# Optimization experiments

Measured on AMD Instinct MI355X. Metric: run time of the kernel, lower is better.

The kernel has to match this reference:

```python
import jax, jax.numpy as jnp
import numpy as np

EMB = 1024
HEADS = 16
HEAD_DIM = EMB // HEADS


def setup_inputs() -> dict:
    key = jax.random.key(0)
    ks = jax.random.split(key, 11)
    B, S = 2, 2048
    scale = 1.0 / np.sqrt(EMB)
    inp = {
        "query": jax.random.normal(ks[0], (B, S, EMB), jnp.float32),
        "key": jax.random.normal(ks[1], (B, S, EMB), jnp.float32),
        "value": jax.random.normal(ks[2], (B, S, EMB), jnp.float32),
        "Wq": jax.random.normal(ks[3], (EMB, EMB), jnp.float32) * scale,
        "bq": jnp.zeros((EMB,), jnp.float32),
        "Wk": jax.random.normal(ks[4], (EMB, EMB), jnp.float32) * scale,
        "bk": jnp.zeros((EMB,), jnp.float32),
        "Wv": jax.random.normal(ks[5], (EMB, EMB), jnp.float32) * scale,
        "bv": jnp.zeros((EMB,), jnp.float32),
        "Wo": jax.random.normal(ks[6], (EMB, EMB), jnp.float32) * scale,
        "bo": jnp.zeros((EMB,), jnp.float32),
    }
    return inp


def reference(query, key, value, Wq, bq, Wk, bk, Wv, bv, Wo, bo):
    B, S, _ = query.shape
    # Linear projections (torch Linear: x @ W.T + b)
    Q = query @ Wq.T + bq
    K = key @ Wk.T + bk
    V = value @ Wv.T + bv
    # [B, H, S, Dh]
    Q = Q.reshape(B, S, HEADS, HEAD_DIM).transpose(0, 2, 1, 3)
    K = K.reshape(B, S, HEADS, HEAD_DIM).transpose(0, 2, 1, 3)
    V = V.reshape(B, S, HEADS, HEAD_DIM).transpose(0, 2, 1, 3)
    scores = jnp.einsum("bhqd,bhkd->bhqk", Q, K) / jnp.sqrt(
        jnp.asarray(HEAD_DIM, Q.dtype)
    )
    attn = jax.nn.softmax(scores, axis=-1)
    ctx = jnp.einsum("bhqk,bhkd->bhqd", attn, V)
    ctx = ctx.transpose(0, 2, 1, 3).reshape(B, S, EMB)
    return ctx @ Wo.T + bo
```

## Files before the change

### kernel.cpp

```cpp
#include <hip/hip_runtime.h>
#include <stdint.h>

typedef __attribute__((ext_vector_type(8)))  __bf16 bf16x8;
typedef __attribute__((ext_vector_type(4)))  float  f32x4;
typedef __attribute__((ext_vector_type(16))) float  f32x16;
typedef __attribute__((ext_vector_type(8)))  ushort u16x8;
typedef __attribute__((ext_vector_type(4)))  ushort u16x4;
typedef __attribute__((ext_vector_type(4)))  uint   u32x4;

#define LOG2E 1.44269504088896f

__device__ __forceinline__ ushort f2bf(float f) {
  uint32_t u = __float_as_uint(f);
  u += 0x7fffu + ((u >> 16) & 1u);
  return (ushort)(u >> 16);
}
__device__ __forceinline__ float bf2f(ushort h) {
  return __uint_as_float(((uint32_t)h) << 16);
}
__device__ __forceinline__ void gload16(const void* g, void* l) {
  __builtin_amdgcn_global_load_lds((const __attribute__((address_space(1))) void*)g,
                                   (__attribute__((address_space(3))) void*)l, 16, 0, 0);
}
__device__ __forceinline__ f32x4 mfma16(bf16x8 a, bf16x8 b, f32x4 c) {
  return __builtin_amdgcn_mfma_f32_16x16x32_bf16(a, b, c, 0, 0, 0);
}
__device__ __forceinline__ f32x16 mfma32(bf16x8 a, bf16x8 b, f32x16 c) {
  return __builtin_amdgcn_mfma_f32_32x32x16_bf16(a, b, c, 0, 0, 0);
}
__device__ __forceinline__ int swz(int row, int byteoff) {
  return row * 128 + (byteoff ^ ((row & 7) << 4));
}
__device__ __forceinline__ uint cvtpk(float lo, float hi) {
  uint w;
  asm("v_cvt_pk_bf16_f32 %0, %1, %2" : "=v"(w) : "v"(lo), "v"(hi));
  return w;
}
__device__ __forceinline__ void plswap(uint& a, uint& b) {
  asm("v_permlane32_swap_b32 %0, %1" : "+v"(a), "+v"(b));
}

struct CvtArgs { const float* src[7]; ushort* dst[7]; };

__global__ __launch_bounds__(256) void cvt_all(CvtArgs a) {
  const int bid = blockIdx.x;
  int seg, base;
  if (bid < 2048) { seg = bid >> 9;              base = bid & 511; }
  else            { seg = 4 + ((bid - 2048) >> 11); base = (bid - 2048) & 2047; }
  const int i = base * 256 + threadIdx.x;
  const f32x4* s = (const f32x4*)a.src[seg];
  f32x4 x = s[2 * i], y = s[2 * i + 1];
  u16x8 o;
  o[0] = f2bf(x[0]); o[1] = f2bf(x[1]); o[2] = f2bf(x[2]); o[3] = f2bf(x[3]);
  o[4] = f2bf(y[0]); o[5] = f2bf(y[1]); o[6] = f2bf(y[2]); o[7] = f2bf(y[3]);
  ((u16x8*)a.dst[seg])[i] = o;
}

struct QKVArgs {
  const ushort* A0; const ushort* A1; const ushort* A2;
  const ushort* W0; const ushort* W1; const ushort* W2;
  const float* b0; const float* b1; const float* b2;
  ushort* Qo; ushort* Ko; ushort* Vo;
};

__global__ __launch_bounds__(256) void qkv_gemm(QKVArgs args) {
  __shared__ ushort Ash[128 * 64];
  __shared__ ushort Bsh[128 * 64];

  const int z = blockIdx.z;
  const ushort* Ab   = z == 0 ? args.A0 : (z == 1 ? args.A1 : args.A2);
  const ushort* Wb   = z == 0 ? args.W0 : (z == 1 ? args.W1 : args.W2);
  const float*  bias = z == 0 ? args.b0 : (z == 1 ? args.b1 : args.b2);

  const int tid = threadIdx.x;
  const int lane = tid & 63, wid = tid >> 6;
  const int l15 = lane & 15, g = lane >> 4;
  const int wr = wid >> 1, wc = wid & 1;
  const int tm = blockIdx.x * 128, tn = blockIdx.y * 128;

  const f32x4 fz = {0.f, 0.f, 0.f, 0.f};
  f32x4 acc[4][4];
#pragma unroll
  for (int m = 0; m < 4; ++m)
#pragma unroll
    for (int n = 0; n < 4; ++n) acc[m][n] = fz;

  const int srow8 = lane >> 3;
  const int ssl   = (lane & 7) ^ srow8;

  for (int kt = 0; kt < 1024; kt += 64) {
#pragma unroll
    for (int c = 0; c < 4; ++c) {
      const int chunk = wid * 4 + c;
      const int row = chunk * 8 + srow8;
      gload16(Wb + (size_t)(tn + row) * 1024 + kt + ssl * 8, &Bsh[chunk * 512]);
      gload16(Ab + (size_t)(tm + row) * 1024 + kt + ssl * 8, &Ash[chunk * 512]);
    }
    __syncthreads();

#pragma unroll
    for (int kk = 0; kk < 2; ++kk) {
      bf16x8 af[4], bfr[4];
#pragma unroll
      for (int m = 0; m < 4; ++m) {
        const int row = wr * 64 + m * 16 + l15;
        af[m] = *(const bf16x8*)&Ash[row * 64 + (((kk * 4 + g) ^ (row & 7)) * 8)];
      }
#pragma unroll
      for (int n = 0; n < 4; ++n) {
        const int row = wc * 64 + n * 16 + l15;
        bfr[n] = *(const bf16x8*)&Bsh[row * 64 + (((kk * 4 + g) ^ (row & 7)) * 8)];
      }
#pragma unroll
      for (int m = 0; m < 4; ++m)
#pragma unroll
        for (int n = 0; n < 4; ++n) acc[m][n] = mfma16(af[m], bfr[n], acc[m][n]);
    }
    __syncthreads();
  }

#pragma unroll
  for (int n = 0; n < 4; ++n) {
    const int col = tn + wc * 64 + n * 16 + l15;
    const float bv = bias[col];
    const int h = col >> 6, d = col & 63;
#pragma unroll
    for (int m = 0; m < 4; ++m) {
      const int row0 = tm + wr * 64 + m * 16 + g * 4;
      if (z == 2) {
        const int b = row0 >> 11, s0 = row0 & 2047;
        u16x4 pk;
#pragma unroll
        for (int r = 0; r < 4; ++r) pk[r] = f2bf(acc[m][n][r] + bv);
        *(u16x4*)&args.Vo[((size_t)((b * 16 + h) * 64 + d)) * 2048 + s0] = pk;
      } else {
        ushort* O = z ? args.Ko : args.Qo;
#pragma unroll
        for (int r = 0; r < 4; ++r) {
          const int row = row0 + r;
          const int b = row >> 11, s = row & 2047;
          O[((size_t)(b * 16 + h) * 2048 + s) * 64 + d] = f2bf(acc[m][n][r] + bv);
        }
      }
    }
  }
}

__global__ __launch_bounds__(256) void attn_fwd(const ushort* __restrict__ Qb,
                                                const ushort* __restrict__ Kb,
                                                const ushort* __restrict__ VTb,
                                                ushort* __restrict__ ctxb) {
  __shared__ char Ksh[64 * 128];
  __shared__ char Vsh[64 * 128];
  __shared__ float Ssc[4][32];

  const int tid = threadIdx.x;
  const int lane = tid & 63, wid = tid >> 6;
  const int l31 = lane & 31, hi = lane >> 5;
  const int bh = blockIdx.y;
  const int q0 = blockIdx.x * 128 + wid * 32;

  const ushort* Qh = Qb + (size_t)bh * 2048 * 64;
  const ushort* Kh = Kb + (size_t)bh * 2048 * 64;
  const ushort* Vh = VTb + (size_t)bh * 64 * 2048;

  bf16x8 qf[4];
  {
    const ushort* qrow = Qh + (size_t)(q0 + l31) * 64;
#pragma unroll
    for (int dt = 0; dt < 4; ++dt) {
      u16x8 raw = *(const u16x8*)&qrow[dt * 16 + hi * 8];
      u16x8 sc;
#pragma unroll
      for (int j = 0; j < 8; ++j) sc[j] = f2bf(bf2f(raw[j]) * 0.125f);
      qf[dt] = __builtin_bit_cast(bf16x8, sc);
    }
  }

  f32x16 o0 = {}, o1 = {};
  float m = -1e30f, lsum = 0.f;

  const int si = tid >> 2, sc4i = tid & 3;
  const ushort* kg = &Kh[(size_t)si * 64 + sc4i * 16];
  const ushort* vg = &Vh[(size_t)si * 2048 + sc4i * 16];

  u16x8 kr0, kr1, vr0, vr1;
  kr0 = *(const u16x8*)kg;  kr1 = *(const u16x8*)(kg + 8);
  vr0 = *(const u16x8*)vg;  vr1 = *(const u16x8*)(vg + 8);
  *(u16x8*)(Ksh + swz(si, sc4i * 32))      = kr0;
  *(u16x8*)(Ksh + swz(si, sc4i * 32 + 16)) = kr1;
  *(u16x8*)(Vsh + swz(si, sc4i * 32))      = vr0;
  *(u16x8*)(Vsh + swz(si, sc4i * 32 + 16)) = vr1;
  __syncthreads();

  for (int t = 0; t < 32; ++t) {
    if (t + 1 < 32) {
      const int kt2 = (t + 1) * 64;
      kr0 = *(const u16x8*)(kg + (size_t)kt2 * 64);
      kr1 = *(const u16x8*)(kg + (size_t)kt2 * 64 + 8);
      vr0 = *(const u16x8*)(vg + kt2);
      vr1 = *(const u16x8*)(vg + kt2 + 8);
    }

    f32x16 P0 = {}, P1 = {};
    __builtin_amdgcn_s_setprio(1);
#pragma unroll
    for (int dt = 0; dt < 4; ++dt) {
      bf16x8 kf0 = *(const bf16x8*)(Ksh + swz(l31,      dt * 32 + hi * 16));
      bf16x8 kf1 = *(const bf16x8*)(Ksh + swz(32 + l31, dt * 32 + hi * 16));
      P0 = mfma32(kf0, qf[dt], P0);
      P1 = mfma32(kf1, qf[dt], P1);
    }
    __builtin_amdgcn_s_setprio(0);

    float pm = fmaxf(P0[0], P1[0]);
#pragma unroll
    for (int r = 1; r + 1 < 16; r += 2) {
      pm = fmaxf(fmaxf(pm, P0[r]), P0[r + 1]);
      pm = fmaxf(fmaxf(pm, P1[r]), P1[r + 1]);
    }
    pm = fmaxf(fmaxf(pm, P0[15]), P1[15]);
    pm = fmaxf(pm, __shfl_xor(pm, 32));

    if (!__all(pm <= m + 8.f)) {
      const float mn = fmaxf(m, pm);
      const float scl = __builtin_amdgcn_exp2f((m - mn) * LOG2E);
      m = mn;
      lsum *= scl;
      Ssc[wid][l31] = scl;
      f32x4 s0 = *(const f32x4*)&Ssc[wid][hi * 4];
      f32x4 s1 = *(const f32x4*)&Ssc[wid][8 + hi * 4];
      f32x4 s2 = *(const f32x4*)&Ssc[wid][16 + hi * 4];
      f32x4 s3 = *(const f32x4*)&Ssc[wid][24 + hi * 4];
#pragma unroll
      for (int r = 0; r < 16; ++r) {
        const float sv = (r < 4 ? s0[r & 3] : r < 8 ? s1[r & 3] : r < 12 ? s2[r & 3] : s3[r & 3]);
        o0[r] *= sv; o1[r] *= sv;
      }
    }

    const float nml = -m * LOG2E;
#pragma unroll
    for (int r = 0; r < 16; ++r)
      P0[r] = __builtin_amdgcn_exp2f(__builtin_fmaf(P0[r], LOG2E, nml));
#pragma unroll
    for (int r = 0; r < 16; ++r)
      P1[r] = __builtin_amdgcn_exp2f(__builtin_fmaf(P1[r], LOG2E, nml));

    float rs = 0.f;
#pragma unroll
    for (int r = 0; r < 16; ++r) rs += P0[r] + P1[r];
    rs += __shfl_xor(rs, 32);
    lsum += rs;

    bf16x8 pa[4];
#pragma unroll
    for (int s = 0; s < 2; ++s) {
      const f32x16& P = s ? P1 : P0;
      uint a0 = cvtpk(P[0], P[1]),  b0 = cvtpk(P[4], P[5]);
      uint a1 = cvtpk(P[2], P[3]),  b1 = cvtpk(P[6], P[7]);
      plswap(a0, b0); plswap(a1, b1);
      pa[2 * s] = __builtin_bit_cast(bf16x8, (u32x4){a0, a1, b0, b1});
      uint a2 = cvtpk(P[8], P[9]),   b2 = cvtpk(P[12], P[13]);
      uint a3 = cvtpk(P[10], P[11]), b3 = cvtpk(P[14], P[15]);
      plswap(a2, b2); plswap(a3, b3);
      pa[2 * s + 1] = __builtin_bit_cast(bf16x8, (u32x4){a2, a3, b2, b3});
    }

    __builtin_amdgcn_s_setprio(1);
#pragma unroll
    for (int kk = 0; kk < 4; ++kk) {
      bf16x8 v0f = *(const bf16x8*)(Vsh + swz(l31,      kk * 32 + hi * 16));
      bf16x8 v1f = *(const bf16x8*)(Vsh + swz(32 + l31, kk * 32 + hi * 16));
      o0 = mfma32(pa[kk], v0f, o0);
      o1 = mfma32(pa[kk], v1f, o1);
    }
    __builtin_amdgcn_s_setprio(0);

    if (t + 1 < 32) {
      __syncthreads();
      *(u16x8*)(Ksh + swz(si, sc4i * 32))      = kr0;
      *(u16x8*)(Ksh + swz(si, sc4i * 32 + 16)) = kr1;
      *(u16x8*)(Vsh + swz(si, sc4i * 32))      = vr0;
      *(u16x8*)(Vsh + swz(si, sc4i * 32 + 16)) = vr1;
      __syncthreads();
    }
  }

  Ssc[wid][l31] = 1.0f / lsum;
  f32x4 i0 = *(const f32x4*)&Ssc[wid][hi * 4];
  f32x4 i1 = *(const f32x4*)&Ssc[wid][8 + hi * 4];
  f32x4 i2 = *(const f32x4*)&Ssc[wid][16 + hi * 4];
  f32x4 i3 = *(const f32x4*)&Ssc[wid][24 + hi * 4];
  const int b = bh >> 4, h = bh & 15;
#pragma unroll
  for (int r = 0; r < 16; ++r) {
    const float inv = (r < 4 ? i0[r & 3] : r < 8 ? i1[r & 3] : r < 12 ? i2[r & 3] : i3[r & 3]);
    const int q = q0 + (r & 3) + 8 * (r >> 2) + 4 * hi;
    const size_t base = ((size_t)(b * 2048 + q)) * 1024 + h * 64;
    ctxb[base + l31]      = f2bf(o0[r] * inv);
    ctxb[base + 32 + l31] = f2bf(o1[r] * inv);
  }
}

__global__ __launch_bounds__(256) void out_gemm(const ushort* __restrict__ A16,
                                                const ushort* __restrict__ Wb,
                                                const float* __restrict__ bias,
                                                float* __restrict__ O) {
  __shared__ ushort Ash[64 * 32];
  __shared__ ushort Bsh[128 * 32];

  const int tid = threadIdx.x;
  const int lane = tid & 63, wid = tid >> 6;
  const int l15 = lane & 15, g = lane >> 4;
  const int wr = wid >> 1, wc = wid & 1;
  const int tm = blockIdx.x * 64, tn = blockIdx.y * 128;

  const f32x4 fz = {0.f, 0.f, 0.f, 0.f};
  f32x4 acc[2][4];
#pragma unroll
  for (int m = 0; m < 2; ++m)
#pragma unroll
    for (int n = 0; n < 4; ++n) acc[m][n] = fz;

  for (int kt = 0; kt < 1024; kt += 32) {
#pragma unroll
    for (int c = 0; c < 2; ++c) {
      const int chunk = wid * 2 + c;
      const int off = chunk * 1024 + lane * 16;
      const int row = off >> 6;
      const int ke = (off & 63) >> 1;
      gload16(Wb + (size_t)(tn + row) * 1024 + kt + ke, &Bsh[chunk * 512]);
    }
    {
      const int off = wid * 1024 + lane * 16;
      const int row = off >> 6;
      const int ke = (off & 63) >> 1;
      gload16(A16 + (size_t)(tm + row) * 1024 + kt + ke, &Ash[wid * 512]);
    }
    __syncthreads();

    bf16x8 af[2], bfr[4];
#pragma unroll
    for (int m = 0; m < 2; ++m)
      af[m] = *(const bf16x8*)&Ash[(wr * 32 + m * 16 + l15) * 32 + g * 8];
#pragma unroll
    for (int n = 0; n < 4; ++n)
      bfr[n] = *(const bf16x8*)&Bsh[(wc * 64 + n * 16 + l15) * 32 + g * 8];
#pragma unroll
    for (int m = 0; m < 2; ++m)
#pragma unroll
      for (int n = 0; n < 4; ++n) acc[m][n] = mfma16(af[m], bfr[n], acc[m][n]);
    __syncthreads();
  }

#pragma unroll
  for (int n = 0; n < 4; ++n) {
    const int col = tn + wc * 64 + n * 16 + l15;
    const float bv = bias[col];
#pragma unroll
    for (int m = 0; m < 2; ++m) {
      const int row0 = tm + wr * 32 + m * 16 + g * 4;
#pragma unroll
      for (int r = 0; r < 4; ++r)
        O[(size_t)(row0 + r) * 1024 + col] = acc[m][n][r] + bv;
    }
  }
}

extern "C" void kernel_launch(void* const* d_in, const int* in_sizes, int n_in,
                              void* d_out, int out_size, void* d_ws, size_t ws_size,
                              hipStream_t stream) {
  const float* query = (const float*)d_in[0];
  const float* key_  = (const float*)d_in[1];
  const float* value = (const float*)d_in[2];
  const float* Wq = (const float*)d_in[3];
  const float* bq = (const float*)d_in[4];
  const float* Wk = (const float*)d_in[5];
  const float* bk = (const float*)d_in[6];
  const float* Wv = (const float*)d_in[7];
  const float* bv = (const float*)d_in[8];
  const float* Wo = (const float*)d_in[9];
  const float* bo = (const float*)d_in[10];

  ushort* ws = (ushort*)d_ws;
  ushort* Wqb = ws;
  ushort* Wkb = ws + (1u << 20);
  ushort* Wvb = ws + (2u << 20);
  ushort* Wob = ws + (3u << 20);
  ushort* Qb  = ws + (4u << 20);
  ushort* Kb  = Qb + (4u << 20);
  ushort* VTb = Kb + (4u << 20);
  ushort* ctx = VTb + (4u << 20);
  ushort* Xqb = ctx;
  ushort* Xkb = (ushort*)d_out;
  ushort* Xvb = (ushort*)d_out + (4u << 20);

  dim3 blk(256);

  CvtArgs ca;
  ca.src[0] = Wq;    ca.dst[0] = Wqb;
  ca.src[1] = Wk;    ca.dst[1] = Wkb;
  ca.src[2] = Wv;    ca.dst[2] = Wvb;
  ca.src[3] = Wo;    ca.dst[3] = Wob;
  ca.src[4] = query; ca.dst[4] = Xqb;
  ca.src[5] = key_;  ca.dst[5] = Xkb;
  ca.src[6] = value; ca.dst[6] = Xvb;
  cvt_all<<<8192, blk, 0, stream>>>(ca);

  QKVArgs a;
  a.A0 = Xqb;  a.A1 = Xkb;  a.A2 = Xvb;
  a.W0 = Wqb;  a.W1 = Wkb;  a.W2 = Wvb;
  a.b0 = bq;   a.b1 = bk;   a.b2 = bv;
  a.Qo = Qb;   a.Ko = Kb;   a.Vo = VTb;
  qkv_gemm<<<dim3(32, 8, 3), blk, 0, stream>>>(a);

  attn_fwd<<<dim3(16, 32), blk, 0, stream>>>(Qb, Kb, VTb, ctx);

  out_gemm<<<dim3(64, 8), blk, 0, stream>>>(ctx, Wob, bo, (float*)d_out);
}
```

Measured before the change: 136.1 us.

## Double-buffer K/V tiles in LDS with direct global-to-LDS async loads

Replaces the register-staged K/V prefetch with global_load_lds direct loads into a double-buffered LDS tile. The next tile is loaded into the alternate buffer while the current one is computed, and the two barriers per iteration become one. This removes register pressure from the staging registers and the LDS write pass, at the cost of twice the LDS footprint. It also depends on the swizzle formula matching what the lane-to-address mapping of the direct loads produces.

New measurement: 140.3 us. 3.1% more time.

```diff
diff --git a/kernel.cpp b/kernel.cpp
--- a/kernel.cpp
+++ b/kernel.cpp
@@ -150,8 +150,8 @@
                                                 const ushort* __restrict__ Kb,
                                                 const ushort* __restrict__ VTb,
                                                 ushort* __restrict__ ctxb) {
-  __shared__ char Ksh[64 * 128];
-  __shared__ char Vsh[64 * 128];
+  __shared__ char Ksh[2][64 * 128];
+  __shared__ char Vsh[2][64 * 128];
   __shared__ float Ssc[4][32];
 
   const int tid = threadIdx.x;
@@ -180,34 +180,35 @@
   f32x16 o0 = {}, o1 = {};
   float m = -1e30f, lsum = 0.f;
 
-  const int si = tid >> 2, sc4i = tid & 3;
-  const ushort* kg = &Kh[(size_t)si * 64 + sc4i * 16];
-  const ushort* vg = &Vh[(size_t)si * 2048 + sc4i * 16];
-
-  u16x8 kr0, kr1, vr0, vr1;
-  kr0 = *(const u16x8*)kg;  kr1 = *(const u16x8*)(kg + 8);
-  vr0 = *(const u16x8*)vg;  vr1 = *(const u16x8*)(vg + 8);
-  *(u16x8*)(Ksh + swz(si, sc4i * 32))      = kr0;
-  *(u16x8*)(Ksh + swz(si, sc4i * 32 + 16)) = kr1;
-  *(u16x8*)(Vsh + swz(si, sc4i * 32))      = vr0;
-  *(u16x8*)(Vsh + swz(si, sc4i * 32 + 16)) = vr1;
+  const int srow8 = lane >> 3;
+  const int ssl   = (lane & 7) ^ srow8;
+
+#define STAGE_KV(buf, kt)                                                     \
+  {                                                                           \
+    _Pragma("unroll")                                                         \
+    for (int c = 0; c < 2; ++c) {                                             \
+      const int chunk = wid * 2 + c;                                          \
+      const int row = chunk * 8 + srow8;                                      \
+      gload16(Kh + (size_t)((kt) + row) * 64 + ssl * 8,                       \
+              &Ksh[buf][chunk * 1024]);                                       \
+      gload16(Vh + (size_t)row * 2048 + (kt) + ssl * 8,                       \
+              &Vsh[buf][chunk * 1024]);                                       \
+    }                                                                         \
+  }
+
+  STAGE_KV(0, 0);
   __syncthreads();
 
   for (int t = 0; t < 32; ++t) {
-    if (t + 1 < 32) {
-      const int kt2 = (t + 1) * 64;
-      kr0 = *(const u16x8*)(kg + (size_t)kt2 * 64);
-      kr1 = *(const u16x8*)(kg + (size_t)kt2 * 64 + 8);
-      vr0 = *(const u16x8*)(vg + kt2);
-      vr1 = *(const u16x8*)(vg + kt2 + 8);
-    }
+    const int cur = t & 1;
+    if (t + 1 < 32) STAGE_KV(cur ^ 1, (t + 1) * 64);
 
     f32x16 P0 = {}, P1 = {};
     __builtin_amdgcn_s_setprio(1);
 #pragma unroll
     for (int dt = 0; dt < 4; ++dt) {
-      bf16x8 kf0 = *(const bf16x8*)(Ksh + swz(l31,      dt * 32 + hi * 16));
-      bf16x8 kf1 = *(const bf16x8*)(Ksh + swz(32 + l31, dt * 32 + hi * 16));
+      bf16x8 kf0 = *(const bf16x8*)(&Ksh[cur][0] + swz(l31,      dt * 32 + hi * 16));
+      bf16x8 kf1 = *(const bf16x8*)(&Ksh[cur][0] + swz(32 + l31, dt * 32 + hi * 16));
       P0 = mfma32(kf0, qf[dt], P0);
       P1 = mfma32(kf1, qf[dt], P1);
     }
@@ -270,22 +271,16 @@
     __builtin_amdgcn_s_setprio(1);
 #pragma unroll
     for (int kk = 0; kk < 4; ++kk) {
-      bf16x8 v0f = *(const bf16x8*)(Vsh + swz(l31,      kk * 32 + hi * 16));
-      bf16x8 v1f = *(const bf16x8*)(Vsh + swz(32 + l31, kk * 32 + hi * 16));
+      bf16x8 v0f = *(const bf16x8*)(&Vsh[cur][0] + swz(l31,      kk * 32 + hi * 16));
+      bf16x8 v1f = *(const bf16x8*)(&Vsh[cur][0] + swz(32 + l31, kk * 32 + hi * 16));
       o0 = mfma32(pa[kk], v0f, o0);
       o1 = mfma32(pa[kk], v1f, o1);
     }
     __builtin_amdgcn_s_setprio(0);
 
-    if (t + 1 < 32) {
-      __syncthreads();
-      *(u16x8*)(Ksh + swz(si, sc4i * 32))      = kr0;
-      *(u16x8*)(Ksh + swz(si, sc4i * 32 + 16)) = kr1;
-      *(u16x8*)(Vsh + swz(si, sc4i * 32))      = vr0;
-      *(u16x8*)(Vsh + swz(si, sc4i * 32 + 16)) = vr1;
-      __syncthreads();
-    }
-  }
+    __syncthreads();
+  }
+#undef STAGE_KV
 
   Ssc[wid][l31] = 1.0f / lsum;
   f32x4 i0 = *(const f32x4*)&Ssc[wid][hi * 4];
```
